# Performance work log

Hardware: AMD Instinct MI355X
Metric: run time of the kernel (lower is better)

Reference implementation:

```python
import jax, jax.numpy as jnp
import numpy as np

L, P, R, A, V, B = 2, 3, 512, 196, 9487, 256


def setup_inputs() -> dict:
    key = jax.random.key(0)
    ks = jax.random.split(key, 20)
    s = 0.02
    inp = {
        "x": jax.random.normal(ks[0], (B, R), jnp.float32),
        "att": jax.random.normal(ks[1], (B, A, R), jnp.float32),
        "inputs": jax.random.normal(ks[2], (2 * L, B, R), jnp.float32),
        # per-layer, per-parallel LSTM core weights (torch Linear: y = x W^T + b)
        "i2h_w": s * jax.random.normal(ks[3], (L, P, 4 * R, R), jnp.float32),
        "i2h_b": s * jax.random.normal(ks[4], (L, P, 4 * R), jnp.float32),
        "h2h_w": s * jax.random.normal(ks[5], (L, P, 4 * R, R), jnp.float32),
        "h2h_b": s * jax.random.normal(ks[6], (L, P, 4 * R), jnp.float32),
        "a2h_w": s * jax.random.normal(ks[7], (L, P, 4 * R, R), jnp.float32),
        "a2h_b": s * jax.random.normal(ks[8], (L, P, 4 * R), jnp.float32),
        # 2 attention modules per layer
        "a2a_w": s * jax.random.normal(ks[9], (L, 2, A, R), jnp.float32),
        "a2a_b": s * jax.random.normal(ks[10], (L, 2, A), jnp.float32),
        "h2a_w": s * jax.random.normal(ks[11], (L, 2, A, R), jnp.float32),
        "h2a_b": s * jax.random.normal(ks[12], (L, 2, A), jnp.float32),
        "d2d_w": s * jax.random.normal(ks[13], (L, 2, A), jnp.float32),
        "d2d_b": s * jax.random.normal(ks[14], (L, 2), jnp.float32),
        "proj_w": s * jax.random.normal(ks[15], (V, R), jnp.float32),
        "proj_b": s * jax.random.normal(ks[16], (V,), jnp.float32),
    }
    return inp


def _soft_att(att, h, a2a_w, a2a_b, h2a_w, h2a_b, d2d_w, d2d_b):
    # att: [B,A,R], h: [B,R]
    v = jnp.einsum('bar,kr->bak', att, a2a_w) + a2a_b          # [B,A,A]
    hh = h @ h2a_w.T + h2a_b                                   # [B,A]
    dot = jnp.tanh(v + hh[:, :, None])                         # [B,A,A]
    score = jnp.einsum('bak,k->ba', dot, d2d_w) + d2d_b        # [B,A]
    w = jax.nn.softmax(score, axis=-1)
    return jnp.einsum('bar,ba->br', att, w)                    # [B,R]


def reference(x, att, inputs, i2h_w, i2h_b, h2h_w, h2h_b, a2h_w, a2h_b,
              a2a_w, a2a_b, h2a_w, h2a_b, d2d_w, d2d_b, proj_w, proj_b):
    outputs = []
    top_h = None
    for i in range(L):
        prev_c = inputs[2 * i]
        prev_h = inputs[2 * i + 1]
        xt = x if i == 0 else x + outputs[-1]
        att_res0 = _soft_att(att, prev_h, a2a_w[i, 0], a2a_b[i, 0],
                             h2a_w[i, 0], h2a_b[i, 0], d2d_w[i, 0], d2d_b[i, 0])
        # fused gates over the P parallel cores: [P,B,4R]
        sums = (jnp.einsum('bi,pgi->pbg', xt, i2h_w[i]) + i2h_b[i][:, None, :]
                + jnp.einsum('bi,pgi->pbg', prev_h, h2h_w[i]) + h2h_b[i][:, None, :]
                + jnp.einsum('bi,pgi->pbg', att_res0, a2h_w[i]) + a2h_b[i][:, None, :])
        sig = jax.nn.sigmoid(sums[..., :3 * R])
        in_g, fg_g, out_g = sig[..., :R], sig[..., R:2 * R], sig[..., 2 * R:3 * R]
        in_t = jnp.tanh(sums[..., 3 * R:])
        nc_p = fg_g * prev_c + in_g * in_t                     # [P,B,R]
        nh_p = out_g * jnp.tanh(nc_p)                          # [P,B,R]
        next_c = nc_p.mean(0)
        next_h = nh_p.mean(0)
        att_res1 = _soft_att(att, next_h, a2a_w[i, 1], a2a_b[i, 1],
                             h2a_w[i, 1], h2a_b[i, 1], d2d_w[i, 1], d2d_b[i, 1])
        top_h = att_res1 + next_h
        outputs.append(next_c)
        outputs.append(top_h)
    logsoft = jax.nn.log_softmax(top_h @ proj_w.T + proj_b, axis=-1)
    return jnp.stack(outputs), logsoft
```

## Files before the change

kernel.cpp:

```cpp
#include <hip/hip_runtime.h>
#include <hip/hip_bf16.h>
#include <math.h>

#define L_ 2
#define P_ 3
#define R_ 512
#define A_ 196
#define V_ 9487
#define B_ 256
#define BR (B_*R_)
#define G4 (4*R_)

typedef short bf16x8 __attribute__((ext_vector_type(8)));
typedef float f32x4  __attribute__((ext_vector_type(4)));
typedef unsigned int u32;

static __device__ __forceinline__ unsigned short f2b(float f){
  u32 u = __builtin_bit_cast(u32, f);
  u += 0x7fffu + ((u >> 16) & 1u);
  return (unsigned short)(u >> 16);
}
static __device__ __forceinline__ float b2f(short s){
  u32 u = ((u32)(unsigned short)s) << 16;
  return __builtin_bit_cast(float, u);
}
static __device__ __forceinline__ bf16x8 cvt8(float4 a, float4 b){
  bf16x8 r;
  r[0]=(short)f2b(a.x); r[1]=(short)f2b(a.y); r[2]=(short)f2b(a.z); r[3]=(short)f2b(a.w);
  r[4]=(short)f2b(b.x); r[5]=(short)f2b(b.y); r[6]=(short)f2b(b.z); r[7]=(short)f2b(b.w);
  return r;
}

static __device__ __forceinline__ void gld16(const void* g, void* l){
  __builtin_amdgcn_global_load_lds(
      (const __attribute__((address_space(1))) u32*)g,
      (__attribute__((address_space(3))) u32*)l, 16, 0, 0);
}

#define SW(x) ((((x)&3) ^ (((x)>>2)&3)))

__global__ __launch_bounds__(256) void k_cvt(const float* __restrict__ src,
                                             short* __restrict__ dst, int n)
{
  const int c = blockIdx.x * 256 + threadIdx.x;
  const int base = c * 8;
  if (base >= n) return;
  float4 a = *(const float4*)(src + base);
  float4 b = *(const float4*)(src + base + 4);
  *(bf16x8*)(dst + base) = cvt8(a, b);
}

__global__ __launch_bounds__(256) void k_cvt_pad_aw(const float* __restrict__ src,
                                                    short* __restrict__ dst)
{
  const int idx8 = (blockIdx.x * 256 + threadIdx.x) * 8;
  const int g   = idx8 >> 17;
  const int rem = idx8 & 131071;
  const int row = rem >> 9;
  const int k   = rem & 511;
  bf16x8 v;
  if (row < A_) {
    const float* sp = src + ((size_t)g * A_ + row) * R_ + k;
    v = cvt8(*(const float4*)sp, *(const float4*)(sp + 4));
  } else {
    v = (bf16x8){0,0,0,0,0,0,0,0};
  }
  *(bf16x8*)(dst + idx8) = v;
}

__global__ __launch_bounds__(256) void k_hh(
    const float* __restrict__ h, const float* __restrict__ hw,
    const float* __restrict__ hb, float* __restrict__ out)
{
  __shared__ float hred[64][5];
  const int t = threadIdx.x;
  const int row = blockIdx.x * 64 + (t >> 2);
  const int seg = t & 3;
  const int b = row / A_;
  const int a = row - b * A_;
  const float* hp = h  + (size_t)b * R_ + seg * 128;
  const float* wp = hw + (size_t)a * R_ + seg * 128;
  float p = 0.f;
#pragma unroll
  for (int k = 0; k < 128; k += 4) {
    float4 a4 = *(const float4*)(hp + k);
    float4 b4 = *(const float4*)(wp + k);
    p = fmaf(a4.x, b4.x, p); p = fmaf(a4.y, b4.y, p);
    p = fmaf(a4.z, b4.z, p); p = fmaf(a4.w, b4.w, p);
  }
  hred[t >> 2][seg] = p;
  __syncthreads();
  if (t < 64) {
    const int m = blockIdx.x * 64 + t;
    const int b2 = m / A_;
    const int a2 = m - b2 * A_;
    out[m] = hred[t][0] + hred[t][1] + hred[t][2] + hred[t][3] + hb[a2];
  }
}

__global__ __launch_bounds__(256) void k_score_mfma(
    const short* __restrict__ att_bf, const short* __restrict__ wbf,
    const float* __restrict__ a2ab, const float* __restrict__ d2dw,
    const float* __restrict__ d2db, const float* __restrict__ hh,
    float* __restrict__ score)
{
  __shared__ __align__(16) short As[2][256 * 8];
  __shared__ __align__(16) short Bs[2][1024 * 8];
  __shared__ float wpad[256], bpad[256], hhs[64], sred[2][64];

  const int t   = threadIdx.x;
  const int m0  = blockIdx.x * 64;
  const int wid = t >> 6, l = t & 63;
  const int wr  = wid >> 1, wc = wid & 1;
  const int q   = l >> 4, lc = l & 15;

  wpad[t] = (t < A_) ? d2dw[t] : 0.f;
  bpad[t] = (t < A_) ? a2ab[t] : 0.f;
  if (t < 64) hhs[t] = hh[m0 + t];

  f32x4 acc[2][8];
#pragma unroll
  for (int i = 0; i < 2; ++i)
#pragma unroll
    for (int j = 0; j < 8; ++j) acc[i][j] = (f32x4){0.f, 0.f, 0.f, 0.f};

  const int a_row  = t >> 2;
  const int a_kb   = (t & 3) ^ SW(a_row);
  const short* a_g = att_bf + (size_t)(m0 + a_row) * R_ + a_kb * 8;
  int b_n[4], b_kb[4];
#pragma unroll
  for (int j = 0; j < 4; ++j) {
    b_n[j]  = j * 64 + (t >> 2);
    b_kb[j] = (t & 3) ^ SW(b_n[j]);
  }

#define STAGE(bufi, kz) {                                                 \
    gld16((const void*)(a_g + (kz)), (void*)&As[bufi][wid * 512]);        \
    _Pragma("unroll")                                                     \
    for (int j = 0; j < 4; ++j)                                           \
      gld16((const void*)(wbf + (size_t)b_n[j] * R_ + (kz) + b_kb[j] * 8),\
            (void*)&Bs[bufi][j * 2048 + wid * 512]);                      \
  }

  STAGE(0, 0);
  __syncthreads();

  for (int ks = 0; ks < 16; ++ks) {
    const int cur = ks & 1;
    if (ks < 15) STAGE(cur ^ 1, (ks + 1) * 32);
    bf16x8 af[2], bfr[8];
#pragma unroll
    for (int mf = 0; mf < 2; ++mf) {
      const int row = wr * 32 + mf * 16 + lc;
      af[mf] = *(const bf16x8*)&As[cur][(row * 4 + (q ^ SW(row))) * 8];
    }
#pragma unroll
    for (int nf = 0; nf < 8; ++nf) {
      const int n = wc * 128 + nf * 16 + lc;
      bfr[nf] = *(const bf16x8*)&Bs[cur][(n * 4 + (q ^ SW(n))) * 8];
    }
#pragma unroll
    for (int mf = 0; mf < 2; ++mf)
#pragma unroll
      for (int nf = 0; nf < 8; ++nf)
        acc[mf][nf] = __builtin_amdgcn_mfma_f32_16x16x32_bf16(af[mf], bfr[nf], acc[mf][nf], 0, 0, 0);
    __syncthreads();
  }
#undef STAGE

  float s[2][4];
#pragma unroll
  for (int mf = 0; mf < 2; ++mf)
#pragma unroll
    for (int r = 0; r < 4; ++r) s[mf][r] = 0.f;

#pragma unroll
  for (int mf = 0; mf < 2; ++mf) {
    const int rbase = wr * 32 + mf * 16 + q * 4;
#pragma unroll
    for (int nf = 0; nf < 8; ++nf) {
      const int col = wc * 128 + nf * 16 + lc;
      const float bp = bpad[col], wp = wpad[col];
#pragma unroll
      for (int r = 0; r < 4; ++r)
        s[mf][r] += tanhf(acc[mf][nf][r] + bp + hhs[rbase + r]) * wp;
    }
  }
#pragma unroll
  for (int mask = 1; mask <= 8; mask <<= 1) {
#pragma unroll
    for (int mf = 0; mf < 2; ++mf)
#pragma unroll
      for (int r = 0; r < 4; ++r) s[mf][r] += __shfl_xor(s[mf][r], mask);
  }
  if (lc == 0) {
#pragma unroll
    for (int mf = 0; mf < 2; ++mf)
#pragma unroll
      for (int r = 0; r < 4; ++r)
        sred[wc][wr * 32 + mf * 16 + q * 4 + r] = s[mf][r];
  }
  __syncthreads();
  if (t < 64) score[m0 + t] = sred[0][t] + sred[1][t] + d2db[0];
}

__global__ __launch_bounds__(256) void k_smax_attres(
    const float* __restrict__ sc, const short* __restrict__ att_bf,
    float* __restrict__ out)
{
  __shared__ float red[256];
  __shared__ float wl[256];
  const int b = blockIdx.x, t = threadIdx.x;
  const float v = (t < A_) ? sc[b * A_ + t] : -INFINITY;
  red[t] = v; __syncthreads();
  for (int s = 128; s > 0; s >>= 1) { if (t < s) red[t] = fmaxf(red[t], red[t+s]); __syncthreads(); }
  const float mx = red[0]; __syncthreads();
  const float e = (t < A_) ? expf(v - mx) : 0.f;
  red[t] = e; __syncthreads();
  for (int s = 128; s > 0; s >>= 1) { if (t < s) red[t] += red[t+s]; __syncthreads(); }
  wl[t] = e / red[0];
  __syncthreads();

  const int r = blockIdx.y * 256 + t;
  const short* ap = att_bf + (size_t)b * A_ * R_ + r;
  float acc = 0.f;
  int a = 0;
#pragma unroll 4
  for (; a < 196; ++a) acc = fmaf(b2f(ap[(size_t)a * R_]), wl[a], acc);
  out[b * R_ + r] = acc;
}

__global__ __launch_bounds__(256) void k_lstm_mfma(
    const float* __restrict__ xt, const float* __restrict__ ph, const float* __restrict__ ar,
    const short* __restrict__ wi, const short* __restrict__ wh, const short* __restrict__ wa,
    int layer, float* __restrict__ sums)
{
  __shared__ __align__(16) short As[4 * 64 * 8];
  __shared__ __align__(16) short Bs[4 * 128 * 8];

  const int t   = threadIdx.x;
  const int m0  = blockIdx.x * 64;
  const int n0  = blockIdx.y * 128;
  const int wid = t >> 6, l = t & 63;
  const int wr  = wid >> 1, wc = wid & 1;
  const int q   = l >> 4, lc = l & 15;

  f32x4 acc[2][4];
#pragma unroll
  for (int i = 0; i < 2; ++i)
#pragma unroll
    for (int j = 0; j < 4; ++j) acc[i][j] = (f32x4){0.f, 0.f, 0.f, 0.f};

  const int s_row = t >> 2, s_kb = t & 3;
  const size_t wrow0 = ((size_t)layer * 6144 + n0) * R_;

  float4 ra0, ra1;
  bf16x8 rb0, rb1;

#define LS_LOAD(ks) {                                                   \
    const int seg = (ks) >> 4;                                          \
    const int kk  = ((ks) & 15) * 32;                                   \
    const float* asel = (seg == 0) ? xt : (seg == 1) ? ph : ar;         \
    const float* ap = asel + (size_t)(m0 + s_row) * R_ + kk + s_kb * 8; \
    ra0 = *(const float4*)ap;                                           \
    ra1 = *(const float4*)(ap + 4);                                     \
    const short* wsel = (seg == 0) ? wi : (seg == 1) ? wh : wa;         \
    const short* bp0 = wsel + wrow0 + (size_t)(s_row      ) * R_ + kk + s_kb * 8; \
    const short* bp1 = wsel + wrow0 + (size_t)(s_row +  64) * R_ + kk + s_kb * 8; \
    rb0 = *(const bf16x8*)bp0;                                          \
    rb1 = *(const bf16x8*)bp1;                                          \
  }
#define LS_STORE() {                                                    \
    *(bf16x8*)&As[s_kb * 512  + s_row * 8] = cvt8(ra0, ra1);            \
    *(bf16x8*)&Bs[s_kb * 1024 + (s_row      ) * 8] = rb0;               \
    *(bf16x8*)&Bs[s_kb * 1024 + (s_row + 64) * 8] = rb1;                \
  }

  LS_LOAD(0);
  for (int ks = 0; ks < 48; ++ks) {
    __syncthreads();
    LS_STORE();
    __syncthreads();
    if (ks < 47) LS_LOAD(ks + 1);
    bf16x8 af[2], bfr[4];
#pragma unroll
    for (int mf = 0; mf < 2; ++mf) {
      const int row = wr * 32 + mf * 16 + lc;
      af[mf] = *(const bf16x8*)&As[q * 512 + row * 8];
    }
#pragma unroll
    for (int nf = 0; nf < 4; ++nf) {
      const int n = wc * 64 + nf * 16 + lc;
      bfr[nf] = *(const bf16x8*)&Bs[q * 1024 + n * 8];
    }
#pragma unroll
    for (int mf = 0; mf < 2; ++mf)
#pragma unroll
      for (int nf = 0; nf < 4; ++nf)
        acc[mf][nf] = __builtin_amdgcn_mfma_f32_16x16x32_bf16(af[mf], bfr[nf], acc[mf][nf], 0, 0, 0);
  }
#undef LS_LOAD
#undef LS_STORE

#pragma unroll
  for (int mf = 0; mf < 2; ++mf) {
#pragma unroll
    for (int nf = 0; nf < 4; ++nf) {
      const int col = n0 + wc * 64 + nf * 16 + lc;
      const int p = col >> 11, g = col & 2047;
#pragma unroll
      for (int r = 0; r < 4; ++r) {
        const int b = m0 + wr * 32 + mf * 16 + q * 4 + r;
        sums[((size_t)p * B_ + b) * (size_t)G4 + g] = acc[mf][nf][r];
      }
    }
  }
}

__global__ __launch_bounds__(256) void k_lstm_elem(
    const float* __restrict__ sums,
    const float* __restrict__ i2hb, const float* __restrict__ h2hb, const float* __restrict__ a2hb,
    const float* __restrict__ prev_c, int layer,
    float* __restrict__ out_c, float* __restrict__ next_h)
{
  const int idx = blockIdx.x * 256 + threadIdx.x;
  const int b = idx >> 9, r = idx & 511;
  const size_t boff = (size_t)layer * P_ * G4;
  const float pc = prev_c[idx];
  float aC = 0.f, aH = 0.f;
#pragma unroll
  for (int p = 0; p < P_; ++p) {
    const float* sp = sums + ((size_t)p * B_ + b) * (size_t)G4;
    const float* b1 = i2hb + boff + p * G4;
    const float* b2 = h2hb + boff + p * G4;
    const float* b3 = a2hb + boff + p * G4;
    const float gi = sp[r]      + b1[r]      + b2[r]      + b3[r];
    const float gf = sp[r+512]  + b1[r+512]  + b2[r+512]  + b3[r+512];
    const float go = sp[r+1024] + b1[r+1024] + b2[r+1024] + b3[r+1024];
    const float gt = sp[r+1536] + b1[r+1536] + b2[r+1536] + b3[r+1536];
    const float ig = 1.f / (1.f + expf(-gi));
    const float fg = 1.f / (1.f + expf(-gf));
    const float og = 1.f / (1.f + expf(-go));
    const float it = tanhf(gt);
    const float nc = fg * pc + ig * it;
    const float nh = og * tanhf(nc);
    aC += nc; aH += nh;
  }
  out_c[idx]  = aC * (1.f/3.f);
  next_h[idx] = aH * (1.f/3.f);
}

__global__ __launch_bounds__(256) void k_toph(
    const float* __restrict__ attres, const float* __restrict__ nh, const float* __restrict__ x,
    float* __restrict__ out_slot, float* __restrict__ toph, float* __restrict__ xt_next, int make_xt)
{
  const int idx = blockIdx.x * 256 + threadIdx.x;
  const float v = attres[idx] + nh[idx];
  out_slot[idx] = v;
  toph[idx] = v;
  if (make_xt) xt_next[idx] = x[idx] + v;
}

__global__ __launch_bounds__(256) void k_proj_mfma(
    const float* __restrict__ th, const short* __restrict__ pwb,
    const float* __restrict__ pb, float* __restrict__ logits)
{
  __shared__ __align__(16) short As[4 * 64 * 8];
  __shared__ __align__(16) short Bs[4 * 128 * 8];

  const int t   = threadIdx.x;
  const int m0  = blockIdx.x * 64;
  const int n0  = blockIdx.y * 128;
  const int wid = t >> 6, l = t & 63;
  const int wr  = wid >> 1, wc = wid & 1;
  const int q   = l >> 4, lc = l & 15;

  f32x4 acc[2][4];
#pragma unroll
  for (int i = 0; i < 2; ++i)
#pragma unroll
    for (int j = 0; j < 4; ++j) acc[i][j] = (f32x4){0.f, 0.f, 0.f, 0.f};

  const int s_row = t >> 2, s_kb = t & 3;
  const int ng0 = n0 + s_row, ng1 = n0 + s_row + 64;

  float4 ra0, ra1;
  bf16x8 rb0, rb1;

#define PJ_LOAD(ks) {                                                   \
    const int kk = (ks) * 32;                                           \
    const float* ap = th + (size_t)(m0 + s_row) * R_ + kk + s_kb * 8;   \
    ra0 = *(const float4*)ap;                                           \
    ra1 = *(const float4*)(ap + 4);                                     \
    if (ng0 < V_) rb0 = *(const bf16x8*)(pwb + (size_t)ng0 * R_ + kk + s_kb * 8); \
    else          rb0 = (bf16x8){0,0,0,0,0,0,0,0};                      \
    if (ng1 < V_) rb1 = *(const bf16x8*)(pwb + (size_t)ng1 * R_ + kk + s_kb * 8); \
    else          rb1 = (bf16x8){0,0,0,0,0,0,0,0};                      \
  }
#define PJ_STORE() {                                                    \
    *(bf16x8*)&As[s_kb * 512  + s_row * 8] = cvt8(ra0, ra1);            \
    *(bf16x8*)&Bs[s_kb * 1024 + (s_row      ) * 8] = rb0;               \
    *(bf16x8*)&Bs[s_kb * 1024 + (s_row + 64) * 8] = rb1;                \
  }

  PJ_LOAD(0);
  for (int ks = 0; ks < 16; ++ks) {
    __syncthreads();
    PJ_STORE();
    __syncthreads();
    if (ks < 15) PJ_LOAD(ks + 1);
    bf16x8 af[2], bfr[4];
#pragma unroll
    for (int mf = 0; mf < 2; ++mf) {
      const int row = wr * 32 + mf * 16 + lc;
      af[mf] = *(const bf16x8*)&As[q * 512 + row * 8];
    }
#pragma unroll
    for (int nf = 0; nf < 4; ++nf) {
      const int n = wc * 64 + nf * 16 + lc;
      bfr[nf] = *(const bf16x8*)&Bs[q * 1024 + n * 8];
    }
#pragma unroll
    for (int mf = 0; mf < 2; ++mf)
#pragma unroll
      for (int nf = 0; nf < 4; ++nf)
        acc[mf][nf] = __builtin_amdgcn_mfma_f32_16x16x32_bf16(af[mf], bfr[nf], acc[mf][nf], 0, 0, 0);
  }
#undef PJ_LOAD
#undef PJ_STORE

#pragma unroll
  for (int mf = 0; mf < 2; ++mf) {
#pragma unroll
    for (int nf = 0; nf < 4; ++nf) {
      const int col = n0 + wc * 64 + nf * 16 + lc;
      if (col < V_) {
        const float bias = pb[col];
#pragma unroll
        for (int r = 0; r < 4; ++r) {
          const int b = m0 + wr * 32 + mf * 16 + q * 4 + r;
          logits[(size_t)b * V_ + col] = acc[mf][nf][r] + bias;
        }
      }
    }
  }
}

__global__ __launch_bounds__(256) void k_logsoftmax(
    const float* __restrict__ logits, float* __restrict__ out)
{
  __shared__ float red[256];
  const int b = blockIdx.x, t = threadIdx.x;
  const float* lp = logits + (size_t)b * V_;
  float mx = -INFINITY;
  for (int n = t; n < V_; n += 256) mx = fmaxf(mx, lp[n]);
  red[t] = mx; __syncthreads();
  for (int s = 128; s > 0; s >>= 1) { if (t < s) red[t] = fmaxf(red[t], red[t+s]); __syncthreads(); }
  mx = red[0]; __syncthreads();
  float sm = 0.f;
  for (int n = t; n < V_; n += 256) sm += expf(lp[n] - mx);
  red[t] = sm; __syncthreads();
  for (int s = 128; s > 0; s >>= 1) { if (t < s) red[t] += red[t+s]; __syncthreads(); }
  const float lse = mx + logf(red[0]);
  float* op = out + (size_t)b * V_;
  for (int n = t; n < V_; n += 256) op[n] = lp[n] - lse;
}

extern "C" void kernel_launch(void* const* d_in, const int* in_sizes, int n_in,
                              void* d_out, int out_size, void* d_ws, size_t ws_size,
                              hipStream_t stream)
{
  const float* x      = (const float*)d_in[0];
  const float* att    = (const float*)d_in[1];
  const float* inputs = (const float*)d_in[2];
  const float* i2hw   = (const float*)d_in[3];
  const float* i2hb   = (const float*)d_in[4];
  const float* h2hw   = (const float*)d_in[5];
  const float* h2hb   = (const float*)d_in[6];
  const float* a2hw   = (const float*)d_in[7];
  const float* a2hb   = (const float*)d_in[8];
  const float* a2aw   = (const float*)d_in[9];
  const float* a2ab   = (const float*)d_in[10];
  const float* h2aw   = (const float*)d_in[11];
  const float* h2ab   = (const float*)d_in[12];
  const float* d2dw   = (const float*)d_in[13];
  const float* d2db   = (const float*)d_in[14];
  const float* pw     = (const float*)d_in[15];
  const float* pb     = (const float*)d_in[16];
  float* out = (float*)d_out;
  float* ws  = (float*)d_ws;

  float* w_score  = ws + 0;
  float* w_hh     = ws + 51200;
  float* w_attres = ws + 102400;
  float* w_xt     = ws + 233472;
  float* w_nexth  = ws + 364544;
  float* w_toph   = ws + 495616;
  float* w_sums   = ws + 626688;
  float* w_logits = ws + 2199552;

  short* bfbase = (short*)(ws + 4628480);
  short* att_bf = bfbase;
  short* awp_bf = bfbase + 25690112;
  short* wi_bf  = bfbase + 26214400;
  short* wh_bf  = bfbase + 32505856;
  short* wa_bf  = bfbase + 38797312;
  short* pw_bf  = bfbase + 45088768;

  k_cvt<<<12544, 256, 0, stream>>>(att, att_bf, 25690112);
  k_cvt_pad_aw<<<256, 256, 0, stream>>>(a2aw, awp_bf);
  k_cvt<<<3072, 256, 0, stream>>>(i2hw, wi_bf, 6291456);
  k_cvt<<<3072, 256, 0, stream>>>(h2hw, wh_bf, 6291456);
  k_cvt<<<3072, 256, 0, stream>>>(a2hw, wa_bf, 6291456);
  k_cvt<<<2372, 256, 0, stream>>>(pw,   pw_bf, 4857344);

  const float* cur_x = x;
  for (int i = 0; i < L_; ++i) {
    const float* prev_c = inputs + (size_t)(2*i)   * BR;
    const float* prev_h = inputs + (size_t)(2*i+1) * BR;

    {
      const int idx = i*2 + 0;
      k_hh<<<784, 256, 0, stream>>>(prev_h, h2aw + (size_t)idx*A_*R_, h2ab + (size_t)idx*A_, w_hh);
      k_score_mfma<<<784, 256, 0, stream>>>(att_bf, awp_bf + (size_t)idx*256*R_,
          a2ab + (size_t)idx*A_, d2dw + (size_t)idx*A_, d2db + idx, w_hh, w_score);
      k_smax_attres<<<dim3(B_, 2), 256, 0, stream>>>(w_score, att_bf, w_attres);
    }

    k_lstm_mfma<<<dim3(4, 48), 256, 0, stream>>>(cur_x, prev_h, w_attres,
                                                 wi_bf, wh_bf, wa_bf, i, w_sums);
    k_lstm_elem<<<512, 256, 0, stream>>>(w_sums, i2hb, h2hb, a2hb, prev_c, i,
                                         out + (size_t)(2*i) * BR, w_nexth);

    {
      const int idx = i*2 + 1;
      k_hh<<<784, 256, 0, stream>>>(w_nexth, h2aw + (size_t)idx*A_*R_, h2ab + (size_t)idx*A_, w_hh);
      k_score_mfma<<<784, 256, 0, stream>>>(att_bf, awp_bf + (size_t)idx*256*R_,
          a2ab + (size_t)idx*A_, d2dw + (size_t)idx*A_, d2db + idx, w_hh, w_score);
      k_smax_attres<<<dim3(B_, 2), 256, 0, stream>>>(w_score, att_bf, w_attres);
    }

    k_toph<<<512, 256, 0, stream>>>(w_attres, w_nexth, x,
                                    out + (size_t)(2*i+1) * BR, w_toph, w_xt,
                                    (i == 0) ? 1 : 0);
    cur_x = w_xt;
  }

  k_proj_mfma<<<dim3(4, 75), 256, 0, stream>>>(w_toph, pw_bf, pb, w_logits);
  k_logsoftmax<<<B_, 256, 0, stream>>>(w_logits, out + (size_t)4 * BR);
}
```

Before: 747.0 us.

## Fuse conversion launches, hh into score, toph into attres, split-K LSTM GEMM

Merges the six conversion kernels into one launch and computes the h2a projection inside the score kernel, so the separate hh kernel goes away. Folds the top_h/x_t update into the softmax-attention kernel, which now has each thread handle two packed bf16 columns with a single block per batch row. Splits the LSTM GEMM over its three input segments along the grid z dimension, writing three partial-sum buffers that the elementwise kernel adds together. This removes several launches and exposes more parallelism, at the cost of extra partial-sum traffic and less parallelism in the attres kernel. When fuse is set, xt is written on both layers even though only the first layer's value is read.

```diff
diff --git a/kernel.cpp b/kernel.cpp
--- a/kernel.cpp
+++ b/kernel.cpp
@@ -10,6 +10,7 @@
 #define B_ 256
 #define BR (B_*R_)
 #define G4 (4*R_)
+#define SSZ 1572864
 
 typedef short bf16x8 __attribute__((ext_vector_type(8)));
 typedef float f32x4  __attribute__((ext_vector_type(4)));
@@ -20,8 +21,8 @@
   u += 0x7fffu + ((u >> 16) & 1u);
   return (unsigned short)(u >> 16);
 }
-static __device__ __forceinline__ float b2f(short s){
-  u32 u = ((u32)(unsigned short)s) << 16;
+static __device__ __forceinline__ float b2f(unsigned short s){
+  u32 u = ((u32)s) << 16;
   return __builtin_bit_cast(float, u);
 }
 static __device__ __forceinline__ bf16x8 cvt8(float4 a, float4 b){
@@ -39,90 +40,70 @@
 
 #define SW(x) ((((x)&3) ^ (((x)>>2)&3)))
 
-__global__ __launch_bounds__(256) void k_cvt(const float* __restrict__ src,
-                                             short* __restrict__ dst, int n)
-{
-  const int c = blockIdx.x * 256 + threadIdx.x;
-  const int base = c * 8;
-  if (base >= n) return;
-  float4 a = *(const float4*)(src + base);
-  float4 b = *(const float4*)(src + base + 4);
-  *(bf16x8*)(dst + base) = cvt8(a, b);
-}
-
-__global__ __launch_bounds__(256) void k_cvt_pad_aw(const float* __restrict__ src,
-                                                    short* __restrict__ dst)
-{
-  const int idx8 = (blockIdx.x * 256 + threadIdx.x) * 8;
-  const int g   = idx8 >> 17;
-  const int rem = idx8 & 131071;
-  const int row = rem >> 9;
-  const int k   = rem & 511;
-  bf16x8 v;
-  if (row < A_) {
-    const float* sp = src + ((size_t)g * A_ + row) * R_ + k;
-    v = cvt8(*(const float4*)sp, *(const float4*)(sp + 4));
+static __device__ __forceinline__ void cvt_range(const float* __restrict__ s,
+                                                 short* __restrict__ d,
+                                                 int lb, int t, int n){
+  const int i8 = (lb * 256 + t) * 8;
+  if (i8 >= n) return;
+  float4 a = *(const float4*)(s + i8);
+  float4 b = *(const float4*)(s + i8 + 4);
+  *(bf16x8*)(d + i8) = cvt8(a, b);
+}
+
+__global__ __launch_bounds__(256) void k_cvt_all(
+    const float* __restrict__ att,  const float* __restrict__ a2aw,
+    const float* __restrict__ i2hw, const float* __restrict__ h2hw,
+    const float* __restrict__ a2hw, const float* __restrict__ pw,
+    short* __restrict__ att_bf, short* __restrict__ awp,
+    short* __restrict__ wi, short* __restrict__ wh,
+    short* __restrict__ wa, short* __restrict__ pwb)
+{
+  const int bid = blockIdx.x, t = threadIdx.x;
+  if (bid < 12544) {
+    cvt_range(att, att_bf, bid, t, 25690112);
+  } else if (bid < 12800) {
+    const int idx8 = ((bid - 12544) * 256 + t) * 8;
+    const int g   = idx8 >> 17;
+    const int rem = idx8 & 131071;
+    const int row = rem >> 9;
+    const int k   = rem & 511;
+    bf16x8 v;
+    if (row < A_) {
+      const float* sp = a2aw + ((size_t)g * A_ + row) * R_ + k;
+      v = cvt8(*(const float4*)sp, *(const float4*)(sp + 4));
+    } else {
+      v = (bf16x8){0,0,0,0,0,0,0,0};
+    }
+    *(bf16x8*)(awp + idx8) = v;
+  } else if (bid < 15872) {
+    cvt_range(i2hw, wi, bid - 12800, t, 6291456);
+  } else if (bid < 18944) {
+    cvt_range(h2hw, wh, bid - 15872, t, 6291456);
+  } else if (bid < 22016) {
+    cvt_range(a2hw, wa, bid - 18944, t, 6291456);
   } else {
-    v = (bf16x8){0,0,0,0,0,0,0,0};
-  }
-  *(bf16x8*)(dst + idx8) = v;
-}
-
-__global__ __launch_bounds__(256) void k_hh(
-    const float* __restrict__ h, const float* __restrict__ hw,
-    const float* __restrict__ hb, float* __restrict__ out)
-{
-  __shared__ float hred[64][5];
-  const int t = threadIdx.x;
-  const int row = blockIdx.x * 64 + (t >> 2);
-  const int seg = t & 3;
-  const int b = row / A_;
-  const int a = row - b * A_;
-  const float* hp = h  + (size_t)b * R_ + seg * 128;
-  const float* wp = hw + (size_t)a * R_ + seg * 128;
-  float p = 0.f;
-#pragma unroll
-  for (int k = 0; k < 128; k += 4) {
-    float4 a4 = *(const float4*)(hp + k);
-    float4 b4 = *(const float4*)(wp + k);
-    p = fmaf(a4.x, b4.x, p); p = fmaf(a4.y, b4.y, p);
-    p = fmaf(a4.z, b4.z, p); p = fmaf(a4.w, b4.w, p);
-  }
-  hred[t >> 2][seg] = p;
-  __syncthreads();
-  if (t < 64) {
-    const int m = blockIdx.x * 64 + t;
-    const int b2 = m / A_;
-    const int a2 = m - b2 * A_;
-    out[m] = hred[t][0] + hred[t][1] + hred[t][2] + hred[t][3] + hb[a2];
+    cvt_range(pw, pwb, bid - 22016, t, 4857344);
   }
 }
 
 __global__ __launch_bounds__(256) void k_score_mfma(
     const short* __restrict__ att_bf, const short* __restrict__ wbf,
     const float* __restrict__ a2ab, const float* __restrict__ d2dw,
-    const float* __restrict__ d2db, const float* __restrict__ hh,
+    const float* __restrict__ d2db,
+    const float* __restrict__ h, const float* __restrict__ h2aw,
+    const float* __restrict__ h2ab,
     float* __restrict__ score)
 {
   __shared__ __align__(16) short As[2][256 * 8];
   __shared__ __align__(16) short Bs[2][1024 * 8];
   __shared__ float wpad[256], bpad[256], hhs[64], sred[2][64];
+  __shared__ float hred[64][4];
 
   const int t   = threadIdx.x;
   const int m0  = blockIdx.x * 64;
   const int wid = t >> 6, l = t & 63;
   const int wr  = wid >> 1, wc = wid & 1;
   const int q   = l >> 4, lc = l & 15;
-
-  wpad[t] = (t < A_) ? d2dw[t] : 0.f;
-  bpad[t] = (t < A_) ? a2ab[t] : 0.f;
-  if (t < 64) hhs[t] = hh[m0 + t];
-
-  f32x4 acc[2][8];
-#pragma unroll
-  for (int i = 0; i < 2; ++i)
-#pragma unroll
-    for (int j = 0; j < 8; ++j) acc[i][j] = (f32x4){0.f, 0.f, 0.f, 0.f};
 
   const int a_row  = t >> 2;
   const int a_kb   = (t & 3) ^ SW(a_row);
@@ -143,7 +124,41 @@
   }
 
   STAGE(0, 0);
+
+  wpad[t] = (t < A_) ? d2dw[t] : 0.f;
+  bpad[t] = (t < A_) ? a2ab[t] : 0.f;
+  {
+    const int hr = t >> 2, hseg = t & 3;
+    const int hm = m0 + hr;
+    const int hb_ = hm / A_;
+    const int ha_ = hm - hb_ * A_;
+    const float* hp = h    + (size_t)hb_ * R_ + hseg * 128;
+    const float* wp = h2aw + (size_t)ha_ * R_ + hseg * 128;
+    float p = 0.f;
+#pragma unroll
+    for (int k = 0; k < 128; k += 4) {
+      float4 a4 = *(const float4*)(hp + k);
+      float4 b4 = *(const float4*)(wp + k);
+      p = fmaf(a4.x, b4.x, p); p = fmaf(a4.y, b4.y, p);
+      p = fmaf(a4.z, b4.z, p); p = fmaf(a4.w, b4.w, p);
+    }
+    hred[hr][hseg] = p;
+  }
+
+  f32x4 acc[2][8];
+#pragma unroll
+  for (int i = 0; i < 2; ++i)
+#pragma unroll
+    for (int j = 0; j < 8; ++j) acc[i][j] = (f32x4){0.f, 0.f, 0.f, 0.f};
+
   __syncthreads();
+
+  if (t < 64) {
+    const int m = m0 + t;
+    const int b2 = m / A_;
+    const int a2 = m - b2 * A_;
+    hhs[t] = hred[t][0] + hred[t][1] + hred[t][2] + hred[t][3] + h2ab[a2];
+  }
 
   for (int ks = 0; ks < 16; ++ks) {
     const int cur = ks & 1;
@@ -206,7 +221,9 @@
 
 __global__ __launch_bounds__(256) void k_smax_attres(
     const float* __restrict__ sc, const short* __restrict__ att_bf,
-    float* __restrict__ out)
+    const float* __restrict__ nh, const float* __restrict__ x,
+    float* __restrict__ attres, float* __restrict__ out_slot,
+    float* __restrict__ toph, float* __restrict__ xt, int fuse)
 {
   __shared__ float red[256];
   __shared__ float wl[256];
@@ -221,19 +238,34 @@
   wl[t] = e / red[0];
   __syncthreads();
 
-  const int r = blockIdx.y * 256 + t;
-  const short* ap = att_bf + (size_t)b * A_ * R_ + r;
-  float acc = 0.f;
-  int a = 0;
+  const int r0 = t * 2;
+  const u32* ap = (const u32*)(att_bf + (size_t)b * A_ * R_ + r0);
+  float acc0 = 0.f, acc1 = 0.f;
 #pragma unroll 4
-  for (; a < 196; ++a) acc = fmaf(b2f(ap[(size_t)a * R_]), wl[a], acc);
-  out[b * R_ + r] = acc;
+  for (int a = 0; a < A_; ++a) {
+    const u32 pk = ap[(size_t)a * 256];
+    const float w = wl[a];
+    acc0 = fmaf(b2f((unsigned short)(pk & 0xffffu)), w, acc0);
+    acc1 = fmaf(b2f((unsigned short)(pk >> 16)),     w, acc1);
+  }
+  const int idx0 = b * R_ + r0;
+  if (!fuse) {
+    attres[idx0]     = acc0;
+    attres[idx0 + 1] = acc1;
+  } else {
+    const float v0 = acc0 + nh[idx0];
+    const float v1 = acc1 + nh[idx0 + 1];
+    out_slot[idx0]     = v0;  out_slot[idx0 + 1] = v1;
+    toph[idx0]         = v0;  toph[idx0 + 1]     = v1;
+    xt[idx0]           = x[idx0] + v0;
+    xt[idx0 + 1]       = x[idx0 + 1] + v1;
+  }
 }
 
 __global__ __launch_bounds__(256) void k_lstm_mfma(
     const float* __restrict__ xt, const float* __restrict__ ph, const float* __restrict__ ar,
     const short* __restrict__ wi, const short* __restrict__ wh, const short* __restrict__ wa,
-    int layer, float* __restrict__ sums)
+    int layer, float* __restrict__ psums)
 {
   __shared__ __align__(16) short As[4 * 64 * 8];
   __shared__ __align__(16) short Bs[4 * 128 * 8];
@@ -241,10 +273,15 @@
   const int t   = threadIdx.x;
   const int m0  = blockIdx.x * 64;
   const int n0  = blockIdx.y * 128;
+  const int z   = blockIdx.z;
   const int wid = t >> 6, l = t & 63;
   const int wr  = wid >> 1, wc = wid & 1;
   const int q   = l >> 4, lc = l & 15;
 
+  const float* asel = (z == 0) ? xt : (z == 1) ? ph : ar;
+  const short* wsel = (z == 0) ? wi : (z == 1) ? wh : wa;
+  const size_t wrow0 = ((size_t)layer * 6144 + n0) * R_;
+
   f32x4 acc[2][4];
 #pragma unroll
   for (int i = 0; i < 2; ++i)
@@ -252,19 +289,15 @@
     for (int j = 0; j < 4; ++j) acc[i][j] = (f32x4){0.f, 0.f, 0.f, 0.f};
 
   const int s_row = t >> 2, s_kb = t & 3;
-  const size_t wrow0 = ((size_t)layer * 6144 + n0) * R_;
 
   float4 ra0, ra1;
   bf16x8 rb0, rb1;
 
 #define LS_LOAD(ks) {                                                   \
-    const int seg = (ks) >> 4;                                          \
-    const int kk  = ((ks) & 15) * 32;                                   \
-    const float* asel = (seg == 0) ? xt : (seg == 1) ? ph : ar;         \
+    const int kk = (ks) * 32;                                           \
     const float* ap = asel + (size_t)(m0 + s_row) * R_ + kk + s_kb * 8; \
     ra0 = *(const float4*)ap;                                           \
     ra1 = *(const float4*)(ap + 4);                                     \
-    const short* wsel = (seg == 0) ? wi : (seg == 1) ? wh : wa;         \
     const short* bp0 = wsel + wrow0 + (size_t)(s_row      ) * R_ + kk + s_kb * 8; \
     const short* bp1 = wsel + wrow0 + (size_t)(s_row +  64) * R_ + kk + s_kb * 8; \
     rb0 = *(const bf16x8*)bp0;                                          \
@@ -277,11 +310,11 @@
   }
 
   LS_LOAD(0);
-  for (int ks = 0; ks < 48; ++ks) {
+  for (int ks = 0; ks < 16; ++ks) {
     __syncthreads();
     LS_STORE();
     __syncthreads();
-    if (ks < 47) LS_LOAD(ks + 1);
+    if (ks < 15) LS_LOAD(ks + 1);
     bf16x8 af[2], bfr[4];
 #pragma unroll
     for (int mf = 0; mf < 2; ++mf) {
@@ -302,6 +335,7 @@
 #undef LS_LOAD
 #undef LS_STORE
 
+  float* zout = psums + (size_t)z * SSZ;
 #pragma unroll
   for (int mf = 0; mf < 2; ++mf) {
 #pragma unroll
@@ -311,14 +345,14 @@
 #pragma unroll
       for (int r = 0; r < 4; ++r) {
         const int b = m0 + wr * 32 + mf * 16 + q * 4 + r;
-        sums[((size_t)p * B_ + b) * (size_t)G4 + g] = acc[mf][nf][r];
+        zout[((size_t)p * B_ + b) * (size_t)G4 + g] = acc[mf][nf][r];
       }
     }
   }
 }
 
 __global__ __launch_bounds__(256) void k_lstm_elem(
-    const float* __restrict__ sums,
+    const float* __restrict__ psums,
     const float* __restrict__ i2hb, const float* __restrict__ h2hb, const float* __restrict__ a2hb,
     const float* __restrict__ prev_c, int layer,
     float* __restrict__ out_c, float* __restrict__ next_h)
@@ -330,14 +364,17 @@
   float aC = 0.f, aH = 0.f;
 #pragma unroll
   for (int p = 0; p < P_; ++p) {
-    const float* sp = sums + ((size_t)p * B_ + b) * (size_t)G4;
+    const size_t base = ((size_t)p * B_ + b) * (size_t)G4;
+    const float* s0 = psums + base;
+    const float* s1 = psums + SSZ + base;
+    const float* s2 = psums + 2 * (size_t)SSZ + base;
     const float* b1 = i2hb + boff + p * G4;
     const float* b2 = h2hb + boff + p * G4;
     const float* b3 = a2hb + boff + p * G4;
-    const float gi = sp[r]      + b1[r]      + b2[r]      + b3[r];
-    const float gf = sp[r+512]  + b1[r+512]  + b2[r+512]  + b3[r+512];
-    const float go = sp[r+1024] + b1[r+1024] + b2[r+1024] + b3[r+1024];
-    const float gt = sp[r+1536] + b1[r+1536] + b2[r+1536] + b3[r+1536];
+    const float gi = s0[r]      + s1[r]      + s2[r]      + b1[r]      + b2[r]      + b3[r];
+    const float gf = s0[r+512]  + s1[r+512]  + s2[r+512]  + b1[r+512]  + b2[r+512]  + b3[r+512];
+    const float go = s0[r+1024] + s1[r+1024] + s2[r+1024] + b1[r+1024] + b2[r+1024] + b3[r+1024];
+    const float gt = s0[r+1536] + s1[r+1536] + s2[r+1536] + b1[r+1536] + b2[r+1536] + b3[r+1536];
     const float ig = 1.f / (1.f + expf(-gi));
     const float fg = 1.f / (1.f + expf(-gf));
     const float og = 1.f / (1.f + expf(-go));
@@ -348,17 +385,6 @@
   }
   out_c[idx]  = aC * (1.f/3.f);
   next_h[idx] = aH * (1.f/3.f);
-}
-
-__global__ __launch_bounds__(256) void k_toph(
-    const float* __restrict__ attres, const float* __restrict__ nh, const float* __restrict__ x,
-    float* __restrict__ out_slot, float* __restrict__ toph, float* __restrict__ xt_next, int make_xt)
-{
-  const int idx = blockIdx.x * 256 + threadIdx.x;
-  const float v = attres[idx] + nh[idx];
-  out_slot[idx] = v;
-  toph[idx] = v;
-  if (make_xt) xt_next[idx] = x[idx] + v;
 }
 
 __global__ __launch_bounds__(256) void k_proj_mfma(
@@ -491,15 +517,14 @@
   float* ws  = (float*)d_ws;
 
   float* w_score  = ws + 0;
-  float* w_hh     = ws + 51200;
-  float* w_attres = ws + 102400;
-  float* w_xt     = ws + 233472;
-  float* w_nexth  = ws + 364544;
-  float* w_toph   = ws + 495616;
-  float* w_sums   = ws + 626688;
-  float* w_logits = ws + 2199552;
-
-  short* bfbase = (short*)(ws + 4628480);
+  float* w_attres = ws + 51200;
+  float* w_xt     = ws + 182272;
+  float* w_nexth  = ws + 313344;
+  float* w_toph   = ws + 444416;
+  float* w_sums3  = ws + 575488;
+  float* w_logits = ws + 5294080;
+
+  short* bfbase = (short*)(ws + 7722752);
   short* att_bf = bfbase;
   short* awp_bf = bfbase + 25690112;
   short* wi_bf  = bfbase + 26214400;
@@ -507,12 +532,8 @@
   short* wa_bf  = bfbase + 38797312;
   short* pw_bf  = bfbase + 45088768;
 
-  k_cvt<<<12544, 256, 0, stream>>>(att, att_bf, 25690112);
-  k_cvt_pad_aw<<<256, 256, 0, stream>>>(a2aw, awp_bf);
-  k_cvt<<<3072, 256, 0, stream>>>(i2hw, wi_bf, 6291456);
-  k_cvt<<<3072, 256, 0, stream>>>(h2hw, wh_bf, 6291456);
-  k_cvt<<<3072, 256, 0, stream>>>(a2hw, wa_bf, 6291456);
-  k_cvt<<<2372, 256, 0, stream>>>(pw,   pw_bf, 4857344);
+  k_cvt_all<<<24388, 256, 0, stream>>>(att, a2aw, i2hw, h2hw, a2hw, pw,
+                                       att_bf, awp_bf, wi_bf, wh_bf, wa_bf, pw_bf);
 
   const float* cur_x = x;
   for (int i = 0; i < L_; ++i) {
@@ -521,28 +542,26 @@
 
     {
       const int idx = i*2 + 0;
-      k_hh<<<784, 256, 0, stream>>>(prev_h, h2aw + (size_t)idx*A_*R_, h2ab + (size_t)idx*A_, w_hh);
       k_score_mfma<<<784, 256, 0, stream>>>(att_bf, awp_bf + (size_t)idx*256*R_,
-          a2ab + (size_t)idx*A_, d2dw + (size_t)idx*A_, d2db + idx, w_hh, w_score);
-      k_smax_attres<<<dim3(B_, 2), 256, 0, stream>>>(w_score, att_bf, w_attres);
-    }
-
-    k_lstm_mfma<<<dim3(4, 48), 256, 0, stream>>>(cur_x, prev_h, w_attres,
-                                                 wi_bf, wh_bf, wa_bf, i, w_sums);
-    k_lstm_elem<<<512, 256, 0, stream>>>(w_sums, i2hb, h2hb, a2hb, prev_c, i,
+          a2ab + (size_t)idx*A_, d2dw + (size_t)idx*A_, d2db + idx,
+          prev_h, h2aw + (size_t)idx*A_*R_, h2ab + (size_t)idx*A_, w_score);
+      k_smax_attres<<<B_, 256, 0, stream>>>(w_score, att_bf,
+          nullptr, nullptr, w_attres, nullptr, nullptr, nullptr, 0);
+    }
+
+    k_lstm_mfma<<<dim3(4, 48, 3), 256, 0, stream>>>(cur_x, prev_h, w_attres,
+                                                    wi_bf, wh_bf, wa_bf, i, w_sums3);
+    k_lstm_elem<<<512, 256, 0, stream>>>(w_sums3, i2hb, h2hb, a2hb, prev_c, i,
                                          out + (size_t)(2*i) * BR, w_nexth);
 
     {
       const int idx = i*2 + 1;
-      k_hh<<<784, 256, 0, stream>>>(w_nexth, h2aw + (size_t)idx*A_*R_, h2ab + (size_t)idx*A_, w_hh);
       k_score_mfma<<<784, 256, 0, stream>>>(att_bf, awp_bf + (size_t)idx*256*R_,
-          a2ab + (size_t)idx*A_, d2dw + (size_t)idx*A_, d2db + idx, w_hh, w_score);
-      k_smax_attres<<<dim3(B_, 2), 256, 0, stream>>>(w_score, att_bf, w_attres);
-    }
-
-    k_toph<<<512, 256, 0, stream>>>(w_attres, w_nexth, x,
-                                    out + (size_t)(2*i+1) * BR, w_toph, w_xt,
-                                    (i == 0) ? 1 : 0);
+          a2ab + (size_t)idx*A_, d2dw + (size_t)idx*A_, d2db + idx,
+          w_nexth, h2aw + (size_t)idx*A_*R_, h2ab + (size_t)idx*A_, w_score);
+      k_smax_attres<<<B_, 256, 0, stream>>>(w_score, att_bf,
+          w_nexth, x, nullptr, out + (size_t)(2*i+1) * BR, w_toph, w_xt, 1);
+    }
     cur_x = w_xt;
   }
 
```

Measured after the change: 700.1 us. 1.07x faster.
